# Kernel tuning notes

Measured on AMD Instinct MI355X. Metric: run time of the kernel, lower is better.

## Reference

```python
import jax, jax.numpy as jnp
import numpy as np


def setup_inputs() -> dict:
    key = jax.random.key(0)
    ks = jax.random.split(key, 9)
    b, m, e, d = 4, 4096, 2048, 256
    s = 1.0 / np.sqrt(d)
    return {
        "features": jax.random.normal(ks[0], (b, m, d), jnp.float32),
        "inc_mat": (jax.random.uniform(ks[1], (b, m, e)) < 0.05).astype(jnp.float32),
        "vc_W_att": jax.random.normal(ks[2], (d, d), jnp.float32) * s,
        "vc_W_proj": jax.random.normal(ks[3], (d, d), jnp.float32) * s,
        "vc_alpha": jnp.float32(0.5),
        "ec_W_att": jax.random.normal(ks[4], (d, d), jnp.float32) * s,
        "ec_W_proj": jax.random.normal(ks[5], (d, d), jnp.float32) * s,
        "ec_alpha": jnp.float32(0.5),
        "n_layers": 3,
    }


def _vertex_conv(feat, inc, W_att, W_proj, alpha, prev_edge):
    # feat: [b,m,d], inc: [b,m,e]
    node_scores = jnp.einsum('bmd,kd->bmk', feat, W_att)          # attention Linear (x @ W.T)
    edge_scores = jnp.einsum('bme,bmd->bed', inc, node_scores)    # inc^T @ scores
    attn = jax.nn.softmax(edge_scores, axis=1)                    # softmax over edge dim (dim=1 in torch)
    # einsum('bme,bmd->bmed') then ('bmed,bed->bed') == attn * (inc^T @ feat); no 4D intermediate
    agg = jnp.einsum('bme,bmd->bed', inc, feat)
    ef = jnp.einsum('bed,kd->bek', attn * agg, W_proj)
    if prev_edge is not None:
        ef = alpha * prev_edge + (1.0 - alpha) * ef
    return ef


def _edge_conv(inc, edge_feats, W_proj, alpha, prev_node):
    # note: EdgeConv's attention softmax is computed but unused in the original forward
    weighted = jnp.einsum('bed,bme->bmd', edge_feats, inc)        # scatter edges back to nodes
    nf = jnp.einsum('bmd,kd->bmk', weighted, W_proj)
    if prev_node is not None:
        nf = alpha * prev_node + (1.0 - alpha) * nf
    return nf


def reference(features, inc_mat, vc_W_att, vc_W_proj, vc_alpha, ec_W_att, ec_W_proj, ec_alpha, n_layers):
    edge_feats = _vertex_conv(features, inc_mat, vc_W_att, vc_W_proj, vc_alpha, None)
    node_feats = _edge_conv(inc_mat, edge_feats, ec_W_proj, ec_alpha, features)
    for _ in range(1, int(n_layers)):
        edge_feats = _vertex_conv(features, inc_mat, vc_W_att, vc_W_proj, vc_alpha, edge_feats)
        node_feats = _edge_conv(inc_mat, edge_feats, ec_W_proj, ec_alpha, node_feats)
    return (node_feats, edge_feats, inc_mat)
```

## Files before the change

### kernel.cpp

```cpp
#include <hip/hip_runtime.h>
#include <hip/hip_bf16.h>
#include <math.h>

typedef __attribute__((ext_vector_type(8))) short s8v;
typedef __attribute__((ext_vector_type(4))) float f32x4;

__device__ __forceinline__ ushort f2bf(float x){ __hip_bfloat16 h = __float2bfloat16(x); return *(ushort*)&h; }
__device__ __forceinline__ float  bf2f(ushort u){ return __bfloat162float(*(__hip_bfloat16*)&u); }

template<int MAP> __device__ __forceinline__ int kmap(int k){
  if constexpr (MAP==0) return k;
  else if constexpr (MAP==1) return k & 4095;
  else if constexpr (MAP==3) return (((k>>8)&1)<<8) | (k&255);
  else if constexpr (MAP==4) return k & 255;
  else return (((k>>9)&1)<<8) | (k&255);
}

template<int AMAP, int BMAP, int EPI, int FR>
__global__ __launch_bounds__(256)
void gemm_kernel(const ushort* __restrict__ A, int lda, long long sA,
                 const ushort* __restrict__ B, int ldb, long long sB,
                 void* __restrict__ Cp, void* __restrict__ Cp2,
                 int ldc, long long sC, long long sC2,
                 long long kpC, long long kpC2,
                 int Kloc, int kparts,
                 const float* __restrict__ blend,
                 const float* __restrict__ alpha_p, const int* __restrict__ L_p)
{
  constexpr int BMt = 32*FR;
  __shared__ ushort As[BMt][40];
  __shared__ ushort Bs[BMt][40];

  const int z  = blockIdx.z;
  const int b  = z / kparts;
  const int kp = z - b*kparts;
  const int kbase = kp * Kloc;
  A += (size_t)b * sA;
  B += (size_t)b * sB;
  const int m0 = blockIdx.x * BMt;
  const int n0 = blockIdx.y * BMt;
  const int t = threadIdx.x, lane = t & 63, wid = t >> 6;
  const int wr = (wid>>1)*(16*FR), wc = (wid&1)*(16*FR);
  const int lrow = lane & 15, koff = (lane>>4)<<3;

  f32x4 acc[FR][FR];
  #pragma unroll
  for (int i=0;i<FR;i++)
    #pragma unroll
    for (int j=0;j<FR;j++) acc[i][j] = (f32x4)(0.f);

  for (int k0 = 0; k0 < Kloc; k0 += 32) {
    if constexpr (FR==4) {
      const int row = t>>1, cb = (t&1)*16;
      { const ushort* s = A + (size_t)(m0+row)*lda + kmap<AMAP>(kbase+k0+cb);
        *(s8v*)&As[row][cb] = *(const s8v*)s; *(s8v*)&As[row][cb+8] = *(const s8v*)(s+8); }
      { const ushort* s = B + (size_t)(n0+row)*ldb + kmap<BMAP>(kbase+k0+cb);
        *(s8v*)&Bs[row][cb] = *(const s8v*)s; *(s8v*)&Bs[row][cb+8] = *(const s8v*)(s+8); }
    } else {
      const int row = t>>2, cb = (t&3)*8;
      *(s8v*)&As[row][cb] = *(const s8v*)(A + (size_t)(m0+row)*lda + kmap<AMAP>(kbase+k0+cb));
      *(s8v*)&Bs[row][cb] = *(const s8v*)(B + (size_t)(n0+row)*ldb + kmap<BMAP>(kbase+k0+cb));
    }
    __syncthreads();
    s8v af[FR], bfv[FR];
    #pragma unroll
    for (int mi=0; mi<FR; mi++) af[mi]  = *(const s8v*)&As[wr+mi*16+lrow][koff];
    #pragma unroll
    for (int ni=0; ni<FR; ni++) bfv[ni] = *(const s8v*)&Bs[wc+ni*16+lrow][koff];
    #pragma unroll
    for (int mi=0; mi<FR; mi++)
      #pragma unroll
      for (int ni=0; ni<FR; ni++)
        acc[mi][ni] = __builtin_amdgcn_mfma_f32_16x16x32_bf16(af[mi], bfv[ni], acc[mi][ni], 0,0,0);
    __syncthreads();
  }

  float aL = 0.f;
  if constexpr (EPI==2) { aL = powf(*alpha_p, (float)(*L_p)); }
  const int cr = (lane>>4)<<2, cc = lane & 15;
  #pragma unroll
  for (int mi=0; mi<FR; mi++)
    #pragma unroll
    for (int ni=0; ni<FR; ni++) {
      const int row0 = m0 + wr + mi*16 + cr;
      const int col  = n0 + wc + ni*16 + cc;
      if constexpr (EPI==5) {
        float* C = (float*)Cp + kp*kpC + (size_t)b*sC;
        #pragma unroll
        for (int r=0;r<4;r++) C[(size_t)(row0+r)*ldc + col] = acc[mi][ni][r];
        if (col < 256) {
          float* C2 = (float*)Cp2 + kp*kpC2 + (size_t)b*sC2 + (size_t)col*2048 + row0;
          *(f32x4*)C2 = acc[mi][ni];
        }
      } else {
        #pragma unroll
        for (int r=0;r<4;r++) {
          const size_t idx = (size_t)b*sC + (size_t)(row0+r)*ldc + col;
          const float v = acc[mi][ni][r];
          if constexpr (EPI==1) ((ushort*)Cp)[idx] = f2bf(v);
          else if constexpr (EPI==2) ((float*)Cp)[idx] = aL*blend[idx] + (1.f-aL)*v;
          else if constexpr (EPI==3) { ((float*)Cp)[idx] = v; ((ushort*)Cp2)[idx] = f2bf(v); }
          else { ushort h = f2bf(v); ((ushort*)Cp)[idx] = h; ((ushort*)Cp2)[idx] = f2bf(v - bf2f(h)); }
        }
      }
    }
}

__global__ __launch_bounds__(256)
void trans_inc_kernel(const float* __restrict__ src, ushort* __restrict__ incbf,
                      ushort* __restrict__ incT)
{
  __shared__ ushort T[64][65];
  const int b = blockIdx.z, m0 = blockIdx.x*64, e0 = blockIdx.y*64;
  const int t = threadIdx.x, rl = t>>2, cl = (t&3)*16;
  const float* s = src + (size_t)b*4096*2048 + (size_t)(m0+rl)*2048 + e0 + cl;
  ushort tmp[16] __attribute__((aligned(16)));
  #pragma unroll
  for (int i=0;i<4;i++) {
    float4 v = ((const float4*)s)[i];
    tmp[4*i+0]=f2bf(v.x); tmp[4*i+1]=f2bf(v.y); tmp[4*i+2]=f2bf(v.z); tmp[4*i+3]=f2bf(v.w);
  }
  ushort* d = incbf + (size_t)b*4096*2048 + (size_t)(m0+rl)*2048 + e0 + cl;
  *(s8v*)d = *(s8v*)&tmp[0]; *(s8v*)(d+8) = *(s8v*)&tmp[8];
  #pragma unroll
  for (int j=0;j<16;j++) T[rl][cl+j] = tmp[j];
  __syncthreads();
  const int er = t>>2, mc = (t&3)*16;
  ushort o[16] __attribute__((aligned(16)));
  #pragma unroll
  for (int j=0;j<16;j++) o[j] = T[mc+j][er];
  ushort* d2 = incT + (size_t)b*2048*4096 + (size_t)(e0+er)*4096 + m0 + mc;
  *(s8v*)d2 = *(s8v*)&o[0]; *(s8v*)(d2+8) = *(s8v*)&o[8];
}

__global__ __launch_bounds__(256)
void trans_feat_kernel(const float* __restrict__ feat, ushort* __restrict__ fcat,
                       ushort* __restrict__ BcatT)
{
  __shared__ ushort Th[64][65], Tl[64][65];
  const int b = blockIdx.z, m0 = blockIdx.x*64, d0 = blockIdx.y*64;
  const int t = threadIdx.x, rl = t>>2, cl = (t&3)*16;
  const float* s = feat + (size_t)b*4096*256 + (size_t)(m0+rl)*256 + d0 + cl;
  ushort hi[16] __attribute__((aligned(16)));
  ushort lo[16] __attribute__((aligned(16)));
  #pragma unroll
  for (int i=0;i<4;i++) {
    float4 v = ((const float4*)s)[i];
    float a[4] = {v.x,v.y,v.z,v.w};
    #pragma unroll
    for (int j=0;j<4;j++) {
      ushort h = f2bf(a[j]); hi[4*i+j] = h; lo[4*i+j] = f2bf(a[j] - bf2f(h));
    }
  }
  ushort* d = fcat + (size_t)b*4096*512 + (size_t)(m0+rl)*512 + d0 + cl;
  *(s8v*)d = *(s8v*)&hi[0]; *(s8v*)(d+8) = *(s8v*)&hi[8];
  *(s8v*)(d+256) = *(s8v*)&lo[0]; *(s8v*)(d+264) = *(s8v*)&lo[8];
  #pragma unroll
  for (int j=0;j<16;j++) { Th[rl][cl+j] = hi[j]; Tl[rl][cl+j] = lo[j]; }
  __syncthreads();
  const int dr = t>>2, mc = (t&3)*16;
  ushort oh[16] __attribute__((aligned(16)));
  ushort ol[16] __attribute__((aligned(16)));
  #pragma unroll
  for (int j=0;j<16;j++) { oh[j] = Th[mc+j][dr]; ol[j] = Tl[mc+j][dr]; }
  ushort* d2 = BcatT + (size_t)b*512*8192 + (size_t)(256+d0+dr)*8192 + m0 + mc;
  *(s8v*)d2 = *(s8v*)&oh[0]; *(s8v*)(d2+8) = *(s8v*)&oh[8];
  *(s8v*)(d2+4096) = *(s8v*)&ol[0]; *(s8v*)(d2+4104) = *(s8v*)&ol[8];
}

__global__ __launch_bounds__(256)
void trans_bf_kernel(const ushort* __restrict__ src, int srcLd, long long srcB,
                     ushort* __restrict__ dst, int dstLd, long long dstB, int colOff)
{
  __shared__ ushort T[64][65];
  const int b = blockIdx.z, r0 = blockIdx.x*64, c0 = blockIdx.y*64;
  const int t = threadIdx.x, rl = t>>2, cl = (t&3)*16;
  const ushort* s = src + (size_t)b*srcB + (size_t)(r0+rl)*srcLd + c0 + cl;
  s8v v0 = *(const s8v*)s, v1 = *(const s8v*)(s+8);
  #pragma unroll
  for (int j=0;j<8;j++) { T[rl][cl+j] = ((const ushort*)&v0)[j]; T[rl][cl+8+j] = ((const ushort*)&v1)[j]; }
  __syncthreads();
  const int cr = t>>2, rc = (t&3)*16;
  ushort o[16] __attribute__((aligned(16)));
  #pragma unroll
  for (int j=0;j<16;j++) o[j] = T[rc+j][cr];
  ushort* d = dst + (size_t)b*dstB + (size_t)(c0+cr)*dstLd + colOff + r0 + rc;
  *(s8v*)d = *(s8v*)&o[0]; *(s8v*)(d+8) = *(s8v*)&o[8];
}

__global__ __launch_bounds__(256)
void cvt_w_kernel(const float4* __restrict__ W, ushort* __restrict__ Ws)
{
  size_t i  = (size_t)blockIdx.x * 256 + threadIdx.x;
  size_t e0 = i * 4;
  int c = (int)(e0 & 255), r = (int)(e0 >> 8);
  float4 v = W[i];
  float a[4] = {v.x,v.y,v.z,v.w};
  ushort* hi = Ws + (size_t)r*512 + c;
  #pragma unroll
  for (int j=0;j<4;j++) { ushort h = f2bf(a[j]); hi[j] = h; hi[256+j] = f2bf(a[j]-bf2f(h)); }
}

__global__ __launch_bounds__(256)
void stats_kernel(const float* __restrict__ ESt, long long kpC2, int kparts,
                  float2* __restrict__ stats)
{
  const int b = blockIdx.x >> 8, d = blockIdx.x & 255;
  const float* base = ESt + (size_t)b*256*2048 + (size_t)d*2048;
  const int t = threadIdx.x;
  float v[8] = {0,0,0,0,0,0,0,0};
  for (int kp=0; kp<kparts; kp++) {
    const float4* p = (const float4*)(base + (size_t)kp*kpC2) + t*2;
    float4 x = p[0], y = p[1];
    v[0]+=x.x; v[1]+=x.y; v[2]+=x.z; v[3]+=x.w;
    v[4]+=y.x; v[5]+=y.y; v[6]+=y.z; v[7]+=y.w;
  }
  float mx = v[0];
  #pragma unroll
  for (int j=1;j<8;j++) mx = fmaxf(mx, v[j]);
  #pragma unroll
  for (int off=32; off>=1; off>>=1) mx = fmaxf(mx, __shfl_down(mx, off));
  __shared__ float sm[8];
  const int lane = t & 63, w = t >> 6;
  if (lane==0) sm[w] = mx;
  __syncthreads();
  if (t==0) { float m = fmaxf(fmaxf(sm[0],sm[1]),fmaxf(sm[2],sm[3])); sm[4] = m; }
  __syncthreads();
  mx = sm[4];
  float s = 0.f;
  #pragma unroll
  for (int j=0;j<8;j++) s += __expf(v[j]-mx);
  #pragma unroll
  for (int off=32; off>=1; off>>=1) s += __shfl_down(s, off);
  if (lane==0) sm[w] = s;
  __syncthreads();
  if (t==0) { float ss = sm[0]+sm[1]+sm[2]+sm[3]; stats[blockIdx.x] = make_float2(mx, 1.f/ss); }
}

__global__ __launch_bounds__(256)
void pmul_kernel(const float* __restrict__ ESAGG, long long kpC, int kparts,
                 const float2* __restrict__ stats, ushort* __restrict__ P)
{
  const int bx = blockIdx.x;
  const int b = bx >> 7, e0 = (bx & 127) * 16;
  const int t = threadIdx.x, er = t >> 4, dc = (t & 15) * 16;
  const int row = e0 + er;
  const size_t base = (size_t)b*2048*512 + (size_t)row*512 + dc;
  float es[16] = {0}, ag[16] = {0};
  for (int kp=0; kp<kparts; kp++) {
    const float4* p = (const float4*)(ESAGG + (size_t)kp*kpC + base);
    const float4* q = p + 64;
    #pragma unroll
    for (int i=0;i<4;i++) {
      float4 a = p[i], c = q[i];
      es[4*i+0]+=a.x; es[4*i+1]+=a.y; es[4*i+2]+=a.z; es[4*i+3]+=a.w;
      ag[4*i+0]+=c.x; ag[4*i+1]+=c.y; ag[4*i+2]+=c.z; ag[4*i+3]+=c.w;
    }
  }
  ushort o[16] __attribute__((aligned(16)));
  #pragma unroll
  for (int j=0;j<16;j++) {
    float2 st = stats[b*256 + dc + j];
    o[j] = f2bf(__expf(es[j]-st.x) * st.y * ag[j]);
  }
  ushort* d = P + (size_t)b*2048*256 + (size_t)row*256 + dc;
  *(s8v*)d = *(s8v*)&o[0]; *(s8v*)(d+8) = *(s8v*)&o[8];
}

__global__ __launch_bounds__(256)
void inc_copy_kernel(const float4* __restrict__ src, float4* __restrict__ dst, size_t n4)
{
  size_t i = (size_t)blockIdx.x*256 + threadIdx.x;
  const size_t stride = (size_t)gridDim.x*256;
  for (; i < n4; i += stride) dst[i] = src[i];
}

extern "C" void kernel_launch(void* const* d_in, const int* in_sizes, int n_in,
                              void* d_out, int out_size, void* d_ws, size_t ws_size,
                              hipStream_t stream) {
  const float* feat    = (const float*)d_in[0];
  const float* inc     = (const float*)d_in[1];
  const float* vcWatt  = (const float*)d_in[2];
  const float* vcWproj = (const float*)d_in[3];
  const float* ecWproj = (const float*)d_in[6];
  const float* ecAlpha = (const float*)d_in[7];
  const int*   nLayers = (const int*)d_in[8];

  const int Bb=4, Mm=4096, E=2048, D=256;
  const size_t nodeN = (size_t)Bb*Mm*D, edgeN = (size_t)Bb*E*D, incN = (size_t)Bb*Mm*E;

  const size_t BcatTB = (size_t)Bb*512*8192*2;
  const size_t fcatB  = (size_t)Bb*4096*512*2;
  const size_t ShB    = nodeN*2, SlB = nodeN*2;
  const size_t PB     = edgeN*2, ebfB = edgeN*2, eTB = edgeN*2;
  const size_t WtB    = nodeN*2;
  const size_t WsB    = (size_t)3*256*512*2;
  const size_t statB  = (size_t)Bb*256*sizeof(float2);
  const size_t fixedB = BcatTB+fcatB+ShB+SlB+PB+ebfB+eTB+WtB+WsB+statB;
  const size_t perKp  = (size_t)Bb*E*512*4 + (size_t)Bb*256*2048*4;
  int kparts = 1;
  if (ws_size >= fixedB + 4*perKp) kparts = 4;
  else if (ws_size >= fixedB + 2*perKp) kparts = 2;

  char* ws = (char*)d_ws;
  ushort* BcatT = (ushort*)ws;                    ws += BcatTB;
  ushort* fcat  = (ushort*)ws;                    ws += fcatB;
  ushort* Sh    = (ushort*)ws;                    ws += ShB;
  ushort* Sl    = (ushort*)ws;                    ws += SlB;
  ushort* P     = (ushort*)ws;                    ws += PB;
  ushort* edgebf= (ushort*)ws;                    ws += ebfB;
  ushort* edgeT = (ushort*)ws;                    ws += eTB;
  ushort* Wt    = (ushort*)ws;                    ws += WtB;
  ushort* Ws0   = (ushort*)ws;
  ushort* Ws1   = Ws0 + 256*512;
  ushort* Ws2   = Ws1 + 256*512;                  ws += WsB;
  float2* stats = (float2*)ws;                    ws += statB;
  float*  ESAGGp= (float*)ws;
  float*  ESt   = ESAGGp + (size_t)kparts*Bb*E*512;

  float* outNode = (float*)d_out;
  float* outEdge = outNode + nodeN;
  float* outInc  = outEdge + edgeN;
  ushort* incT  = (ushort*)outInc;
  ushort* incbf = incT + (size_t)Bb*2048*4096;

  const long long kpC  = (long long)Bb*E*512;
  const long long kpC2 = (long long)Bb*256*2048;
  dim3 blk(256);

  cvt_w_kernel<<<dim3(64), blk, 0, stream>>>((const float4*)vcWatt,  Ws0);
  cvt_w_kernel<<<dim3(64), blk, 0, stream>>>((const float4*)vcWproj, Ws1);
  cvt_w_kernel<<<dim3(64), blk, 0, stream>>>((const float4*)ecWproj, Ws2);
  trans_feat_kernel<<<dim3(64,4,4), blk, 0, stream>>>(feat, fcat, BcatT);
  trans_inc_kernel<<<dim3(64,32,4), blk, 0, stream>>>(inc, incbf, incT);

  gemm_kernel<5,3,4,2><<<dim3(64,4,4), blk, 0, stream>>>(
      fcat, 512, (long long)Mm*512, Ws0, 512, 0,
      Sh, Sl, D, (long long)Mm*D, 0, 0, 0, 1024, 1, nullptr, nullptr, nullptr);
  trans_bf_kernel<<<dim3(64,4,4), blk, 0, stream>>>(Sh, 256, (long long)Mm*D, BcatT, 8192, (long long)512*8192, 0);
  trans_bf_kernel<<<dim3(64,4,4), blk, 0, stream>>>(Sl, 256, (long long)Mm*D, BcatT, 8192, (long long)512*8192, 4096);

  gemm_kernel<1,0,5,4><<<dim3(16,4,4*kparts), blk, 0, stream>>>(
      incT, 4096, (long long)E*4096, BcatT, 8192, (long long)512*8192,
      ESAGGp, ESt, 512, (long long)E*512, (long long)256*2048,
      kpC, kpC2, 8192/kparts, kparts, nullptr, nullptr, nullptr);

  stats_kernel<<<dim3(Bb*256), blk, 0, stream>>>(ESt, kpC2, kparts, stats);
  pmul_kernel<<<dim3(Bb*128), blk, 0, stream>>>(ESAGGp, kpC, kparts, stats, P);

  gemm_kernel<4,3,3,2><<<dim3(32,4,4), blk, 0, stream>>>(
      P, 256, (long long)E*D, Ws1, 512, 0,
      outEdge, edgebf, D, (long long)E*D, 0, 0, 0, 512, 1, nullptr, nullptr, nullptr);
  trans_bf_kernel<<<dim3(32,4,4), blk, 0, stream>>>(edgebf, 256, (long long)E*D, edgeT, 2048, (long long)256*2048, 0);

  gemm_kernel<0,0,1,2><<<dim3(64,4,4), blk, 0, stream>>>(
      incbf, 2048, (long long)Mm*E, edgeT, 2048, (long long)256*2048,
      Wt, nullptr, D, (long long)Mm*D, 0, 0, 0, 2048, 1, nullptr, nullptr, nullptr);

  gemm_kernel<4,3,2,2><<<dim3(64,4,4), blk, 0, stream>>>(
      Wt, 256, (long long)Mm*D, Ws2, 512, 0,
      outNode, nullptr, D, (long long)Mm*D, 0, 0, 0, 512, 1, feat, ecAlpha, nLayers);

  inc_copy_kernel<<<dim3(2048), blk, 0, stream>>>((const float4*)inc, (float4*)outInc, incN/4);
}
```

Measured before the change: 607.9 us.

## Reassociate attention scores as (inc^T feat) W_att and fuse inc copy into transpose

Edge scores are now computed by first aggregating features over edges (inc^T @ feat, a single N=256 GEMM with split-K over 8 parts), then projecting with W_att on the much smaller edge tensor. This replaces the node-level score GEMM and its two transposes, and halves the N width of the large incidence GEMM. The GEMM epilogues now write transposed outputs directly, which removes the separate bf16 transpose kernels. When the workspace is large enough, the fp32 incidence copy to the output is folded into the transpose kernel, so one full read of the incidence matrix is skipped. The cost is an extra reduction kernel over the split-K parts and possible precision drift from the reordered products.

```diff
diff --git a/kernel.cpp b/kernel.cpp
--- a/kernel.cpp
+++ b/kernel.cpp
@@ -21,9 +21,8 @@
 void gemm_kernel(const ushort* __restrict__ A, int lda, long long sA,
                  const ushort* __restrict__ B, int ldb, long long sB,
                  void* __restrict__ Cp, void* __restrict__ Cp2,
-                 int ldc, long long sC, long long sC2,
-                 long long kpC, long long kpC2,
-                 int Kloc, int kparts,
+                 int ldc, long long sC, int ldc2, long long sC2,
+                 long long kpC, int Kloc, int kparts,
                  const float* __restrict__ blend,
                  const float* __restrict__ alpha_p, const int* __restrict__ L_p)
 {
@@ -84,43 +83,63 @@
     for (int ni=0; ni<FR; ni++) {
       const int row0 = m0 + wr + mi*16 + cr;
       const int col  = n0 + wc + ni*16 + cc;
-      if constexpr (EPI==5) {
+      if constexpr (EPI==0) {
         float* C = (float*)Cp + kp*kpC + (size_t)b*sC;
         #pragma unroll
         for (int r=0;r<4;r++) C[(size_t)(row0+r)*ldc + col] = acc[mi][ni][r];
-        if (col < 256) {
-          float* C2 = (float*)Cp2 + kp*kpC2 + (size_t)b*sC2 + (size_t)col*2048 + row0;
-          *(f32x4*)C2 = acc[mi][ni];
+      } else if constexpr (EPI==1) {
+        ushort* C = (ushort*)Cp + (size_t)b*sC;
+        #pragma unroll
+        for (int r=0;r<4;r++) C[(size_t)(row0+r)*ldc + col] = f2bf(acc[mi][ni][r]);
+      } else if constexpr (EPI==2) {
+        float* C = (float*)Cp + (size_t)b*sC;
+        const float* bl = blend + (size_t)b*sC;
+        #pragma unroll
+        for (int r=0;r<4;r++) {
+          const size_t idx = (size_t)(row0+r)*ldc + col;
+          C[idx] = aL*bl[idx] + (1.f-aL)*acc[mi][ni][r];
         }
+      } else if constexpr (EPI==6) {
+        float* C = (float*)Cp + (size_t)b*sC;
+        #pragma unroll
+        for (int r=0;r<4;r++) C[(size_t)(row0+r)*ldc + col] = acc[mi][ni][r];
+        float* C2 = (float*)Cp2 + (size_t)b*sC2 + (size_t)col*ldc2 + row0;
+        *(f32x4*)C2 = acc[mi][ni];
       } else {
-        #pragma unroll
-        for (int r=0;r<4;r++) {
-          const size_t idx = (size_t)b*sC + (size_t)(row0+r)*ldc + col;
-          const float v = acc[mi][ni][r];
-          if constexpr (EPI==1) ((ushort*)Cp)[idx] = f2bf(v);
-          else if constexpr (EPI==2) ((float*)Cp)[idx] = aL*blend[idx] + (1.f-aL)*v;
-          else if constexpr (EPI==3) { ((float*)Cp)[idx] = v; ((ushort*)Cp2)[idx] = f2bf(v); }
-          else { ushort h = f2bf(v); ((ushort*)Cp)[idx] = h; ((ushort*)Cp2)[idx] = f2bf(v - bf2f(h)); }
-        }
+        float* C = (float*)Cp + (size_t)b*sC;
+        #pragma unroll
+        for (int r=0;r<4;r++) C[(size_t)(row0+r)*ldc + col] = acc[mi][ni][r];
+        ushort4 o;
+        o.x = f2bf(acc[mi][ni][0]); o.y = f2bf(acc[mi][ni][1]);
+        o.z = f2bf(acc[mi][ni][2]); o.w = f2bf(acc[mi][ni][3]);
+        *(ushort4*)((ushort*)Cp2 + (size_t)b*sC2 + (size_t)col*ldc2 + row0) = o;
       }
     }
 }
 
 __global__ __launch_bounds__(256)
-void trans_inc_kernel(const float* __restrict__ src, ushort* __restrict__ incbf,
-                      ushort* __restrict__ incT)
+void trans_inc_kernel(const float* __restrict__ src, float* __restrict__ outF32, int writeF32,
+                      ushort* __restrict__ incbf, ushort* __restrict__ incT)
 {
   __shared__ ushort T[64][65];
   const int b = blockIdx.z, m0 = blockIdx.x*64, e0 = blockIdx.y*64;
   const int t = threadIdx.x, rl = t>>2, cl = (t&3)*16;
-  const float* s = src + (size_t)b*4096*2048 + (size_t)(m0+rl)*2048 + e0 + cl;
+  const size_t roff = (size_t)b*4096*2048 + (size_t)(m0+rl)*2048 + e0 + cl;
+  const float* s = src + roff;
   ushort tmp[16] __attribute__((aligned(16)));
+  float4 vv[4];
   #pragma unroll
   for (int i=0;i<4;i++) {
-    float4 v = ((const float4*)s)[i];
-    tmp[4*i+0]=f2bf(v.x); tmp[4*i+1]=f2bf(v.y); tmp[4*i+2]=f2bf(v.z); tmp[4*i+3]=f2bf(v.w);
-  }
-  ushort* d = incbf + (size_t)b*4096*2048 + (size_t)(m0+rl)*2048 + e0 + cl;
+    vv[i] = ((const float4*)s)[i];
+    tmp[4*i+0]=f2bf(vv[i].x); tmp[4*i+1]=f2bf(vv[i].y);
+    tmp[4*i+2]=f2bf(vv[i].z); tmp[4*i+3]=f2bf(vv[i].w);
+  }
+  if (writeF32) {
+    float4* o = (float4*)(outF32 + roff);
+    #pragma unroll
+    for (int i=0;i<4;i++) o[i] = vv[i];
+  }
+  ushort* d = incbf + roff;
   *(s8v*)d = *(s8v*)&tmp[0]; *(s8v*)(d+8) = *(s8v*)&tmp[8];
   #pragma unroll
   for (int j=0;j<16;j++) T[rl][cl+j] = tmp[j];
@@ -134,58 +153,30 @@
 }
 
 __global__ __launch_bounds__(256)
-void trans_feat_kernel(const float* __restrict__ feat, ushort* __restrict__ fcat,
-                       ushort* __restrict__ BcatT)
+void trans_feat_kernel(const float* __restrict__ feat, ushort* __restrict__ fT)
 {
   __shared__ ushort Th[64][65], Tl[64][65];
   const int b = blockIdx.z, m0 = blockIdx.x*64, d0 = blockIdx.y*64;
   const int t = threadIdx.x, rl = t>>2, cl = (t&3)*16;
   const float* s = feat + (size_t)b*4096*256 + (size_t)(m0+rl)*256 + d0 + cl;
-  ushort hi[16] __attribute__((aligned(16)));
-  ushort lo[16] __attribute__((aligned(16)));
   #pragma unroll
   for (int i=0;i<4;i++) {
     float4 v = ((const float4*)s)[i];
     float a[4] = {v.x,v.y,v.z,v.w};
     #pragma unroll
     for (int j=0;j<4;j++) {
-      ushort h = f2bf(a[j]); hi[4*i+j] = h; lo[4*i+j] = f2bf(a[j] - bf2f(h));
+      ushort h = f2bf(a[j]); Th[rl][cl+4*i+j] = h; Tl[rl][cl+4*i+j] = f2bf(a[j] - bf2f(h));
     }
   }
-  ushort* d = fcat + (size_t)b*4096*512 + (size_t)(m0+rl)*512 + d0 + cl;
-  *(s8v*)d = *(s8v*)&hi[0]; *(s8v*)(d+8) = *(s8v*)&hi[8];
-  *(s8v*)(d+256) = *(s8v*)&lo[0]; *(s8v*)(d+264) = *(s8v*)&lo[8];
-  #pragma unroll
-  for (int j=0;j<16;j++) { Th[rl][cl+j] = hi[j]; Tl[rl][cl+j] = lo[j]; }
   __syncthreads();
   const int dr = t>>2, mc = (t&3)*16;
   ushort oh[16] __attribute__((aligned(16)));
   ushort ol[16] __attribute__((aligned(16)));
   #pragma unroll
   for (int j=0;j<16;j++) { oh[j] = Th[mc+j][dr]; ol[j] = Tl[mc+j][dr]; }
-  ushort* d2 = BcatT + (size_t)b*512*8192 + (size_t)(256+d0+dr)*8192 + m0 + mc;
+  ushort* d2 = fT + (size_t)b*256*8192 + (size_t)(d0+dr)*8192 + m0 + mc;
   *(s8v*)d2 = *(s8v*)&oh[0]; *(s8v*)(d2+8) = *(s8v*)&oh[8];
   *(s8v*)(d2+4096) = *(s8v*)&ol[0]; *(s8v*)(d2+4104) = *(s8v*)&ol[8];
-}
-
-__global__ __launch_bounds__(256)
-void trans_bf_kernel(const ushort* __restrict__ src, int srcLd, long long srcB,
-                     ushort* __restrict__ dst, int dstLd, long long dstB, int colOff)
-{
-  __shared__ ushort T[64][65];
-  const int b = blockIdx.z, r0 = blockIdx.x*64, c0 = blockIdx.y*64;
-  const int t = threadIdx.x, rl = t>>2, cl = (t&3)*16;
-  const ushort* s = src + (size_t)b*srcB + (size_t)(r0+rl)*srcLd + c0 + cl;
-  s8v v0 = *(const s8v*)s, v1 = *(const s8v*)(s+8);
-  #pragma unroll
-  for (int j=0;j<8;j++) { T[rl][cl+j] = ((const ushort*)&v0)[j]; T[rl][cl+8+j] = ((const ushort*)&v1)[j]; }
-  __syncthreads();
-  const int cr = t>>2, rc = (t&3)*16;
-  ushort o[16] __attribute__((aligned(16)));
-  #pragma unroll
-  for (int j=0;j<16;j++) o[j] = T[rc+j][cr];
-  ushort* d = dst + (size_t)b*dstB + (size_t)(c0+cr)*dstLd + colOff + r0 + rc;
-  *(s8v*)d = *(s8v*)&o[0]; *(s8v*)(d+8) = *(s8v*)&o[8];
 }
 
 __global__ __launch_bounds__(256)
@@ -202,19 +193,37 @@
 }
 
 __global__ __launch_bounds__(256)
-void stats_kernel(const float* __restrict__ ESt, long long kpC2, int kparts,
-                  float2* __restrict__ stats)
+void aggsum_kernel(const float* __restrict__ parts, long long kpC, int kparts,
+                   ushort* __restrict__ AGGcat)
+{
+  const size_t i4 = (size_t)blockIdx.x*256 + threadIdx.x;
+  float4 sv = make_float4(0.f,0.f,0.f,0.f);
+  for (int kp=0; kp<kparts; kp++) {
+    float4 v = ((const float4*)(parts + (size_t)kp*kpC))[i4];
+    sv.x+=v.x; sv.y+=v.y; sv.z+=v.z; sv.w+=v.w;
+  }
+  const size_t flat = i4*4;
+  const size_t row = flat >> 8;
+  const int d = (int)(flat & 255);
+  float a[4] = {sv.x, sv.y, sv.z, sv.w};
+  ushort4 hi, lo;
+  { ushort h=f2bf(a[0]); hi.x=h; lo.x=f2bf(a[0]-bf2f(h)); }
+  { ushort h=f2bf(a[1]); hi.y=h; lo.y=f2bf(a[1]-bf2f(h)); }
+  { ushort h=f2bf(a[2]); hi.z=h; lo.z=f2bf(a[2]-bf2f(h)); }
+  { ushort h=f2bf(a[3]); hi.w=h; lo.w=f2bf(a[3]-bf2f(h)); }
+  ushort* dst = AGGcat + row*512 + d;
+  *(ushort4*)dst = hi; *(ushort4*)(dst+256) = lo;
+}
+
+__global__ __launch_bounds__(256)
+void stats_kernel(const float* __restrict__ ESt, float2* __restrict__ stats)
 {
   const int b = blockIdx.x >> 8, d = blockIdx.x & 255;
-  const float* base = ESt + (size_t)b*256*2048 + (size_t)d*2048;
+  const float* base = ESt + ((size_t)b*256 + d)*2048;
   const int t = threadIdx.x;
-  float v[8] = {0,0,0,0,0,0,0,0};
-  for (int kp=0; kp<kparts; kp++) {
-    const float4* p = (const float4*)(base + (size_t)kp*kpC2) + t*2;
-    float4 x = p[0], y = p[1];
-    v[0]+=x.x; v[1]+=x.y; v[2]+=x.z; v[3]+=x.w;
-    v[4]+=y.x; v[5]+=y.y; v[6]+=y.z; v[7]+=y.w;
-  }
+  const float4* p = (const float4*)base + t*2;
+  float4 x = p[0], y = p[1];
+  float v[8] = {x.x,x.y,x.z,x.w,y.x,y.y,y.z,y.w};
   float mx = v[0];
   #pragma unroll
   for (int j=1;j<8;j++) mx = fmaxf(mx, v[j]);
@@ -224,7 +233,7 @@
   const int lane = t & 63, w = t >> 6;
   if (lane==0) sm[w] = mx;
   __syncthreads();
-  if (t==0) { float m = fmaxf(fmaxf(sm[0],sm[1]),fmaxf(sm[2],sm[3])); sm[4] = m; }
+  if (t==0) { sm[4] = fmaxf(fmaxf(sm[0],sm[1]),fmaxf(sm[2],sm[3])); }
   __syncthreads();
   mx = sm[4];
   float s = 0.f;
@@ -238,33 +247,26 @@
 }
 
 __global__ __launch_bounds__(256)
-void pmul_kernel(const float* __restrict__ ESAGG, long long kpC, int kparts,
+void pmul_kernel(const float* __restrict__ ES, const ushort* __restrict__ AGGcat,
                  const float2* __restrict__ stats, ushort* __restrict__ P)
 {
-  const int bx = blockIdx.x;
-  const int b = bx >> 7, e0 = (bx & 127) * 16;
-  const int t = threadIdx.x, er = t >> 4, dc = (t & 15) * 16;
-  const int row = e0 + er;
-  const size_t base = (size_t)b*2048*512 + (size_t)row*512 + dc;
-  float es[16] = {0}, ag[16] = {0};
-  for (int kp=0; kp<kparts; kp++) {
-    const float4* p = (const float4*)(ESAGG + (size_t)kp*kpC + base);
-    const float4* q = p + 64;
-    #pragma unroll
-    for (int i=0;i<4;i++) {
-      float4 a = p[i], c = q[i];
-      es[4*i+0]+=a.x; es[4*i+1]+=a.y; es[4*i+2]+=a.z; es[4*i+3]+=a.w;
-      ag[4*i+0]+=c.x; ag[4*i+1]+=c.y; ag[4*i+2]+=c.z; ag[4*i+3]+=c.w;
-    }
-  }
-  ushort o[16] __attribute__((aligned(16)));
-  #pragma unroll
-  for (int j=0;j<16;j++) {
-    float2 st = stats[b*256 + dc + j];
-    o[j] = f2bf(__expf(es[j]-st.x) * st.y * ag[j]);
-  }
-  ushort* d = P + (size_t)b*2048*256 + (size_t)row*256 + dc;
-  *(s8v*)d = *(s8v*)&o[0]; *(s8v*)(d+8) = *(s8v*)&o[8];
+  const int b = blockIdx.x >> 6, e0 = (blockIdx.x & 63) * 32;
+  const int t = threadIdx.x, tx = t & 63, ty = t >> 6;
+  const int d4 = tx*4;
+  const float2 st0 = stats[b*256+d4+0], st1 = stats[b*256+d4+1];
+  const float2 st2 = stats[b*256+d4+2], st3 = stats[b*256+d4+3];
+  for (int e = e0+ty; e < e0+32; e += 4) {
+    const size_t ro = (size_t)b*2048 + e;
+    float4 es = *(const float4*)(ES + ro*256 + d4);
+    ushort4 ah = *(const ushort4*)(AGGcat + ro*512 + d4);
+    ushort4 al = *(const ushort4*)(AGGcat + ro*512 + 256 + d4);
+    ushort4 o;
+    o.x = f2bf(__expf(es.x-st0.x)*st0.y*(bf2f(ah.x)+bf2f(al.x)));
+    o.y = f2bf(__expf(es.y-st1.x)*st1.y*(bf2f(ah.y)+bf2f(al.y)));
+    o.z = f2bf(__expf(es.z-st2.x)*st2.y*(bf2f(ah.z)+bf2f(al.z)));
+    o.w = f2bf(__expf(es.w-st3.x)*st3.y*(bf2f(ah.w)+bf2f(al.w)));
+    *(ushort4*)(P + ro*256 + d4) = o;
+  }
 }
 
 __global__ __launch_bounds__(256)
@@ -289,77 +291,82 @@
   const int Bb=4, Mm=4096, E=2048, D=256;
   const size_t nodeN = (size_t)Bb*Mm*D, edgeN = (size_t)Bb*E*D, incN = (size_t)Bb*Mm*E;
 
-  const size_t BcatTB = (size_t)Bb*512*8192*2;
-  const size_t fcatB  = (size_t)Bb*4096*512*2;
-  const size_t ShB    = nodeN*2, SlB = nodeN*2;
-  const size_t PB     = edgeN*2, ebfB = edgeN*2, eTB = edgeN*2;
+  const int kparts = 8;
+  const size_t fTB    = (size_t)Bb*256*8192*2;
+  const size_t partsB = (size_t)kparts*Bb*E*D*4;
+  const size_t AGGcatB= (size_t)Bb*E*512*2;
+  const size_t ESB    = (size_t)Bb*E*D*4;
+  const size_t EStB   = ESB;
+  const size_t PB     = edgeN*2;
+  const size_t edgeTB = edgeN*2;
   const size_t WtB    = nodeN*2;
   const size_t WsB    = (size_t)3*256*512*2;
   const size_t statB  = (size_t)Bb*256*sizeof(float2);
-  const size_t fixedB = BcatTB+fcatB+ShB+SlB+PB+ebfB+eTB+WtB+WsB+statB;
-  const size_t perKp  = (size_t)Bb*E*512*4 + (size_t)Bb*256*2048*4;
-  int kparts = 1;
-  if (ws_size >= fixedB + 4*perKp) kparts = 4;
-  else if (ws_size >= fixedB + 2*perKp) kparts = 2;
+  const size_t incTB  = incN*2, incbfB = incN*2;
+  const size_t needB  = fTB+partsB+AGGcatB+ESB+EStB+PB+edgeTB+WtB+WsB+statB;
+  const bool planA = ws_size >= needB + incTB + incbfB;
 
   char* ws = (char*)d_ws;
-  ushort* BcatT = (ushort*)ws;                    ws += BcatTB;
-  ushort* fcat  = (ushort*)ws;                    ws += fcatB;
-  ushort* Sh    = (ushort*)ws;                    ws += ShB;
-  ushort* Sl    = (ushort*)ws;                    ws += SlB;
-  ushort* P     = (ushort*)ws;                    ws += PB;
-  ushort* edgebf= (ushort*)ws;                    ws += ebfB;
-  ushort* edgeT = (ushort*)ws;                    ws += eTB;
-  ushort* Wt    = (ushort*)ws;                    ws += WtB;
+  ushort* fT    = (ushort*)ws;  ws += fTB;
+  float*  parts = (float*)ws;   ws += partsB;
+  ushort* AGGcat= (ushort*)ws;  ws += AGGcatB;
+  float*  ES    = (float*)ws;   ws += ESB;
+  float*  ESt   = (float*)ws;   ws += EStB;
+  ushort* P     = (ushort*)ws;  ws += PB;
+  ushort* edgeT = (ushort*)ws;  ws += edgeTB;
+  ushort* Wt    = (ushort*)ws;  ws += WtB;
   ushort* Ws0   = (ushort*)ws;
   ushort* Ws1   = Ws0 + 256*512;
-  ushort* Ws2   = Ws1 + 256*512;                  ws += WsB;
-  float2* stats = (float2*)ws;                    ws += statB;
-  float*  ESAGGp= (float*)ws;
-  float*  ESt   = ESAGGp + (size_t)kparts*Bb*E*512;
+  ushort* Ws2   = Ws1 + 256*512;
+  ws += WsB;
+  float2* stats = (float2*)ws;  ws += statB;
 
   float* outNode = (float*)d_out;
   float* outEdge = outNode + nodeN;
   float* outInc  = outEdge + edgeN;
-  ushort* incT  = (ushort*)outInc;
-  ushort* incbf = incT + (size_t)Bb*2048*4096;
-
-  const long long kpC  = (long long)Bb*E*512;
-  const long long kpC2 = (long long)Bb*256*2048;
+  ushort* incT, *incbf;
+  if (planA) { incT = (ushort*)ws; incbf = incT + incN; }
+  else       { incT = (ushort*)outInc; incbf = incT + incN; }
+
+  const long long kpC = (long long)Bb*E*D;
   dim3 blk(256);
 
   cvt_w_kernel<<<dim3(64), blk, 0, stream>>>((const float4*)vcWatt,  Ws0);
   cvt_w_kernel<<<dim3(64), blk, 0, stream>>>((const float4*)vcWproj, Ws1);
   cvt_w_kernel<<<dim3(64), blk, 0, stream>>>((const float4*)ecWproj, Ws2);
-  trans_feat_kernel<<<dim3(64,4,4), blk, 0, stream>>>(feat, fcat, BcatT);
-  trans_inc_kernel<<<dim3(64,32,4), blk, 0, stream>>>(inc, incbf, incT);
-
-  gemm_kernel<5,3,4,2><<<dim3(64,4,4), blk, 0, stream>>>(
-      fcat, 512, (long long)Mm*512, Ws0, 512, 0,
-      Sh, Sl, D, (long long)Mm*D, 0, 0, 0, 1024, 1, nullptr, nullptr, nullptr);
-  trans_bf_kernel<<<dim3(64,4,4), blk, 0, stream>>>(Sh, 256, (long long)Mm*D, BcatT, 8192, (long long)512*8192, 0);
-  trans_bf_kernel<<<dim3(64,4,4), blk, 0, stream>>>(Sl, 256, (long long)Mm*D, BcatT, 8192, (long long)512*8192, 4096);
-
-  gemm_kernel<1,0,5,4><<<dim3(16,4,4*kparts), blk, 0, stream>>>(
-      incT, 4096, (long long)E*4096, BcatT, 8192, (long long)512*8192,
-      ESAGGp, ESt, 512, (long long)E*512, (long long)256*2048,
-      kpC, kpC2, 8192/kparts, kparts, nullptr, nullptr, nullptr);
-
-  stats_kernel<<<dim3(Bb*256), blk, 0, stream>>>(ESt, kpC2, kparts, stats);
-  pmul_kernel<<<dim3(Bb*128), blk, 0, stream>>>(ESAGGp, kpC, kparts, stats, P);
-
-  gemm_kernel<4,3,3,2><<<dim3(32,4,4), blk, 0, stream>>>(
+  trans_feat_kernel<<<dim3(64,4,4), blk, 0, stream>>>(feat, fT);
+  trans_inc_kernel<<<dim3(64,32,4), blk, 0, stream>>>(inc, outInc, planA ? 1 : 0, incbf, incT);
+
+  gemm_kernel<1,0,0,4><<<dim3(16,2,4*kparts), blk, 0, stream>>>(
+      incT, 4096, (long long)E*4096, fT, 8192, (long long)256*8192,
+      parts, nullptr, D, (long long)E*D, 0, 0, kpC, 8192/kparts, kparts,
+      nullptr, nullptr, nullptr);
+
+  aggsum_kernel<<<dim3(2048), blk, 0, stream>>>(parts, kpC, kparts, AGGcat);
+
+  gemm_kernel<5,3,6,2><<<dim3(32,4,4), blk, 0, stream>>>(
+      AGGcat, 512, (long long)E*512, Ws0, 512, 0,
+      ES, ESt, D, (long long)E*D, E, (long long)D*E, 0, 1024, 1,
+      nullptr, nullptr, nullptr);
+
+  stats_kernel<<<dim3(Bb*256), blk, 0, stream>>>(ESt, stats);
+  pmul_kernel<<<dim3(Bb*64), blk, 0, stream>>>(ES, AGGcat, stats, P);
+
+  gemm_kernel<4,3,7,2><<<dim3(32,4,4), blk, 0, stream>>>(
       P, 256, (long long)E*D, Ws1, 512, 0,
-      outEdge, edgebf, D, (long long)E*D, 0, 0, 0, 512, 1, nullptr, nullptr, nullptr);
-  trans_bf_kernel<<<dim3(32,4,4), blk, 0, stream>>>(edgebf, 256, (long long)E*D, edgeT, 2048, (long long)256*2048, 0);
+      outEdge, edgeT, D, (long long)E*D, E, (long long)D*E, 0, 512, 1,
+      nullptr, nullptr, nullptr);
 
   gemm_kernel<0,0,1,2><<<dim3(64,4,4), blk, 0, stream>>>(
-      incbf, 2048, (long long)Mm*E, edgeT, 2048, (long long)256*2048,
-      Wt, nullptr, D, (long long)Mm*D, 0, 0, 0, 2048, 1, nullptr, nullptr, nullptr);
+      incbf, 2048, (long long)Mm*E, edgeT, 2048, (long long)D*E,
+      Wt, nullptr, D, (long long)Mm*D, 0, 0, 0, 2048, 1,
+      nullptr, nullptr, nullptr);
 
   gemm_kernel<4,3,2,2><<<dim3(64,4,4), blk, 0, stream>>>(
       Wt, 256, (long long)Mm*D, Ws2, 512, 0,
-      outNode, nullptr, D, (long long)Mm*D, 0, 0, 0, 512, 1, feat, ecAlpha, nLayers);
-
-  inc_copy_kernel<<<dim3(2048), blk, 0, stream>>>((const float4*)inc, (float4*)outInc, incN/4);
-}
+      outNode, nullptr, D, (long long)Mm*D, 0, 0, 0, 512, 1,
+      feat, ecAlpha, nLayers);
+
+  if (!planA)
+    inc_copy_kernel<<<dim3(2048), blk, 0, stream>>>((const float4*)inc, (float4*)outInc, incN/4);
+}
```

New measurement: 527.5 us. -13.2%, faster.
